# Kernel optimization log

Measured on AMD Instinct MI355X. Metric: run time of the kernel, lower is better.

## Reference

```python
import jax, jax.numpy as jnp
import numpy as np

E = 1024       # embed_dim
H = 16         # num_heads
HD = E // H    # head_dim = 64
ROPE = 32      # qk_rope_head_dim
NOPE = HD - ROPE  # 32
QR = 512       # q_lora_rank
KVR = 512      # kv_lora_rank
B, S = 1, 4096
EPS = 1e-5


def setup_inputs() -> dict:
    key = jax.random.key(0)
    ks = jax.random.split(key, 10)
    std = 0.02
    x = jax.random.normal(ks[0], (B, S, E), dtype=jnp.float32)
    mask = jnp.tril(jnp.ones((S, S), dtype=jnp.int32))  # causal decoder mask
    Wqa = jax.random.normal(ks[1], (QR, E), dtype=jnp.float32) * std
    qa_ln_w = jnp.ones((QR,), jnp.float32) + jax.random.normal(ks[2], (QR,), jnp.float32) * 0.01
    qa_ln_b = jax.random.normal(ks[3], (QR,), jnp.float32) * 0.01
    Wqb = jax.random.normal(ks[4], (H * HD, QR), dtype=jnp.float32) * std
    Wkva = jax.random.normal(ks[5], (KVR + ROPE, E), dtype=jnp.float32) * std
    kva_ln_w = jnp.ones((KVR,), jnp.float32) + jax.random.normal(ks[6], (KVR,), jnp.float32) * 0.01
    kva_ln_b = jax.random.normal(ks[7], (KVR,), jnp.float32) * 0.01
    Wkvb = jax.random.normal(ks[8], (H * (NOPE + HD), KVR), dtype=jnp.float32) * std
    Wo = jax.random.normal(ks[9], (E, H * HD), dtype=jnp.float32) * std
    return {"x": x, "mask": mask, "Wqa": Wqa, "qa_ln_w": qa_ln_w, "qa_ln_b": qa_ln_b,
            "Wqb": Wqb, "Wkva": Wkva, "kva_ln_w": kva_ln_w, "kva_ln_b": kva_ln_b,
            "Wkvb": Wkvb, "Wo": Wo}


def _layernorm(x, w, b):
    mu = jnp.mean(x, axis=-1, keepdims=True)
    var = jnp.var(x, axis=-1, keepdims=True)
    return (x - mu) * jax.lax.rsqrt(var + EPS) * w + b


def _rope_freqs(seq_len):
    inv_freq = 1.0 / (10000.0 ** (jnp.arange(0, ROPE, 2, dtype=jnp.float32) / ROPE))
    freqs = jnp.arange(seq_len, dtype=jnp.float32)[:, None] * inv_freq[None, :]  # [S, ROPE/2]
    return jnp.cos(freqs), jnp.sin(freqs)


def _apply_rope(x, cos, sin):
    # x: [B, S, h, ROPE] (interleaved-pair RoPE). cos/sin: [S, ROPE/2]
    x1 = x[..., ::2]
    x2 = x[..., 1::2]
    c = cos[None, :, None, :]
    s = sin[None, :, None, :]
    r1 = x1 * c - x2 * s
    r2 = x1 * s + x2 * c
    return jnp.stack([r1, r2], axis=-1).reshape(x.shape)


def reference(x, mask, Wqa, qa_ln_w, qa_ln_b, Wqb, Wkva, kva_ln_w, kva_ln_b, Wkvb, Wo):
    b, s, _ = x.shape
    # Q LoRA path
    q_c = _layernorm(x @ Wqa.T, qa_ln_w, qa_ln_b)          # [B,S,QR]
    q = (q_c @ Wqb.T).reshape(b, s, H, HD)                 # [B,S,H,HD]
    q_nope, q_pe = q[..., :NOPE], q[..., NOPE:]
    # KV LoRA path with decoupled rope channel
    kv = x @ Wkva.T                                        # [B,S,KVR+ROPE]
    ckv, k_pe = kv[..., :KVR], kv[..., KVR:]
    ckv = _layernorm(ckv, kva_ln_w, kva_ln_b)
    kv_dec = (ckv @ Wkvb.T).reshape(b, s, H, NOPE + HD)    # [B,S,H,NOPE+HD]
    k_nope, v = kv_dec[..., :NOPE], kv_dec[..., NOPE:]
    k_pe = k_pe.reshape(b, s, 1, ROPE)
    cos, sin = _rope_freqs(s)
    q_pe = _apply_rope(q_pe, cos, sin)
    k_pe = _apply_rope(k_pe, cos, sin)
    q_full = jnp.concatenate([q_nope, q_pe], axis=-1)      # [B,S,H,HD]
    k_full = jnp.concatenate([k_nope, jnp.broadcast_to(k_pe, (b, s, H, ROPE))], axis=-1)
    scale = 1.0 / np.sqrt(HD)
    scores = jnp.einsum('bqhd,bkhd->bhqk', q_full, k_full) * scale
    scores = jnp.where(mask[None, None, :, :] == 0, jnp.float32(-1e9), scores)
    p = jax.nn.softmax(scores, axis=-1)                    # dropout is identity (eval)
    out = jnp.einsum('bhqk,bkhd->bqhd', p, v).reshape(b, s, H * HD)
    return out @ Wo.T
```

## Files before the change

kernel.cpp:

```cpp
#include <hip/hip_runtime.h>
#include <hip/hip_bf16.h>
#include <stdint.h>


#define SLEN 4096
#define EDIM 1024
#define NH   16
#define NPAIR 160

typedef __attribute__((ext_vector_type(8))) short short8;
typedef __attribute__((ext_vector_type(4))) float f32x4;

__device__ __forceinline__ ushort f2bf(float f) {
  __hip_bfloat16 h = __float2bfloat16(f);
  ushort u; __builtin_memcpy(&u, &h, 2); return u;
}
__device__ __forceinline__ float bf2f(ushort u) {
  uint32_t x = (uint32_t)u << 16;
  float f; __builtin_memcpy(&f, &x, 4); return f;
}
__device__ __forceinline__ uint32_t cvt_pk_bf16(float lo, float hi) {
  uint32_t r;
  asm("v_cvt_pk_bf16_f32 %0, %1, %2" : "=v"(r) : "v"(lo), "v"(hi));
  return r;
}

#define GLD_LDS16(g, l) __builtin_amdgcn_global_load_lds(                      \
    (const __attribute__((address_space(1))) uint32_t*)(g),                    \
    (__attribute__((address_space(3))) uint32_t*)(l), 16, 0, 0)

struct CastSeg { const float4* src; ushort* dst; int n4; };
struct CastArgs { CastSeg seg[6]; int total4; };
__global__ void cast_all(CastArgs a) {
  int i = blockIdx.x * blockDim.x + threadIdx.x;
  int stride = gridDim.x * blockDim.x;
  for (; i < a.total4; i += stride) {
    int idx = i, s = 0;
    while (idx >= a.seg[s].n4) { idx -= a.seg[s].n4; ++s; }
    float4 v = a.seg[s].src[idx];
    ushort4 o;
    o.x = f2bf(v.x); o.y = f2bf(v.y); o.z = f2bf(v.z); o.w = f2bf(v.w);
    *(ushort4*)(a.seg[s].dst + (size_t)idx * 4) = o;
  }
}

__global__ void rope_table(float* __restrict__ cosT, float* __restrict__ sinT) {
  int idx = blockIdx.x * blockDim.x + threadIdx.x;
  if (idx >= SLEN * 16) return;
  int s = idx >> 4, i = idx & 15;
  float inv = expf(-((float)(2 * i) / 32.0f) * logf(10000.0f));
  float ang = (float)s * inv;
  cosT[idx] = cosf(ang);
  sinT[idx] = sinf(ang);
}

template <typename CT, bool ROPE, bool KVPACK>
__device__ __forceinline__ void gemm_body(
    ushort* As, ushort* Bs,
    const ushort* __restrict__ A, const ushort* __restrict__ B, CT* __restrict__ C,
    int M, int N, int K, int bx, int by,
    const float* __restrict__ cosT, const float* __restrict__ sinT,
    ushort* __restrict__ kf, ushort* __restrict__ vt) {
  const int tid = threadIdx.x;
  const int lane = tid & 63, wave = tid >> 6;
  const int bm = bx * 64, bn = by * 128;
  const int wm = (wave >> 1) * 32, wn = (wave & 1) * 64;

  f32x4 acc[2][4];
#pragma unroll
  for (int m = 0; m < 2; ++m)
#pragma unroll
    for (int n = 0; n < 4; ++n) acc[m][n] = (f32x4)0.0f;

  const int srow = lane >> 3;
  const int scb = (lane & 7) << 4;
  const int srcb = scb ^ ((srow & 7) << 4);

  auto stage = [&](int k0, int buf) {
#pragma unroll
    for (int c = 0; c < 2; ++c) {
      int r = wave * 16 + c * 8 + srow;
      const ushort* ga = A + (size_t)(bm + r) * K + k0 + (srcb >> 1);
      GLD_LDS16(ga, As + buf * 4096 + (wave * 16 + c * 8) * 64);
    }
#pragma unroll
    for (int c = 0; c < 4; ++c) {
      int r = wave * 32 + c * 8 + srow;
      int rb = bn + r; if (rb >= N) rb = N - 1;
      const ushort* gb = B + (size_t)rb * K + k0 + (srcb >> 1);
      GLD_LDS16(gb, Bs + buf * 8192 + (wave * 32 + c * 8) * 64);
    }
  };

  stage(0, 0);
  __syncthreads();
  int cur = 0;
  for (int k0 = 0; k0 < K; k0 += 64) {
    if (k0 + 64 < K) stage(k0 + 64, cur ^ 1);
    const char* Ab = (const char*)(As + cur * 4096);
    const char* Bb = (const char*)(Bs + cur * 8192);
#pragma unroll
    for (int kk = 0; kk < 2; ++kk) {
      short8 af[2], bf[4];
#pragma unroll
      for (int m = 0; m < 2; ++m) {
        int row = wm + m * 16 + (lane & 15);
        int cb = (kk * 64 + ((lane >> 4) << 4)) ^ ((row & 7) << 4);
        af[m] = *(const short8*)(Ab + row * 128 + cb);
      }
#pragma unroll
      for (int n = 0; n < 4; ++n) {
        int row = wn + n * 16 + (lane & 15);
        int cb = (kk * 64 + ((lane >> 4) << 4)) ^ ((row & 7) << 4);
        bf[n] = *(const short8*)(Bb + row * 128 + cb);
      }
#pragma unroll
      for (int m = 0; m < 2; ++m)
#pragma unroll
        for (int n = 0; n < 4; ++n)
          acc[m][n] = __builtin_amdgcn_mfma_f32_16x16x32_bf16(af[m], bf[n], acc[m][n], 0, 0, 0);
    }
    __syncthreads();
    cur ^= 1;
  }

  if constexpr (KVPACK) {
    ushort* T = Bs;
#pragma unroll
    for (int m = 0; m < 2; ++m) {
      int gm = bm + wm + m * 16 + ((lane >> 4) << 2);
#pragma unroll
      for (int n = 0; n < 4; ++n) {
        int gn = bn + wn + n * 16 + (lane & 15);
        int h = gn / 96, dd = gn - h * 96;
#pragma unroll
        for (int r = 0; r < 4; ++r) {
          float v = acc[m][n][r];
          int s = gm + r;
          if (dd < 32) {
            kf[(size_t)s * EDIM + h * 64 + dd] = f2bf(v);
          } else {
            int so = s & 63;
            int sp = ((so >> 4) & 1) * 32 + ((so >> 2) & 3) * 8 + ((so >> 5) & 1) * 4 + (so & 3);
            T[(gn - bn) * 68 + sp] = f2bf(v);
          }
        }
      }
    }
    __syncthreads();
    int c = tid >> 1, half = tid & 1;
    int gn2 = bn + c, h2 = gn2 / 96, dd2 = gn2 - h2 * 96;
    if (dd2 >= 32) {
      ushort* dst = vt + (size_t)(h2 * 64 + dd2 - 32) * SLEN + bm + half * 32;
      const ushort* src = T + c * 68 + half * 32;
#pragma unroll
      for (int j = 0; j < 32; j += 4)
        *(ushort4*)(dst + j) = *(const ushort4*)(src + j);
    }
  } else {
    const float SCQ = 0.125f * 1.44269504089f;
#pragma unroll
    for (int m = 0; m < 2; ++m) {
      int gm = bm + wm + m * 16 + ((lane >> 4) << 2);
#pragma unroll
      for (int n = 0; n < 4; ++n) {
        int gn = bn + wn + n * 16 + (lane & 15);
        if (gn < N) {
#pragma unroll
          for (int r = 0; r < 4; ++r) {
            float v = acc[m][n][r];
            if constexpr (ROPE) {
              float partner = __shfl_xor(v, 1);
              int d = gn & 63;
              if (d >= 32) {
                int s = gm + r, pidx = (d - 32) >> 1;
                float cc = cosT[(s << 4) + pidx], sn = sinT[(s << 4) + pidx];
                v = (gn & 1) ? (partner * sn + v * cc) : (v * cc - partner * sn);
              }
              v *= SCQ;
            }
            if constexpr (__is_same(CT, ushort))
              C[(size_t)(gm + r) * N + gn] = f2bf(v);
            else
              C[(size_t)(gm + r) * N + gn] = v;
          }
        }
      }
    }
  }
}

__global__ __launch_bounds__(256, 3) void gemm_f32k(
    const ushort* __restrict__ A, const ushort* __restrict__ B, float* __restrict__ C,
    int M, int N, int K) {
  __shared__ ushort As[2 * 64 * 64];
  __shared__ ushort Bs[2 * 128 * 64];
  gemm_body<float, false, false>(As, Bs, A, B, C, M, N, K, blockIdx.x, blockIdx.y,
                                 nullptr, nullptr, nullptr, nullptr);
}
__global__ __launch_bounds__(256, 3) void gemm_bf16k(
    const ushort* __restrict__ A, const ushort* __restrict__ B, ushort* __restrict__ C,
    int M, int N, int K) {
  __shared__ ushort As[2 * 64 * 64];
  __shared__ ushort Bs[2 * 128 * 64];
  gemm_body<ushort, false, false>(As, Bs, A, B, C, M, N, K, blockIdx.x, blockIdx.y,
                                  nullptr, nullptr, nullptr, nullptr);
}
__global__ __launch_bounds__(256, 3) void gemm_dual(
    const ushort* __restrict__ Aq, const ushort* __restrict__ Bq, ushort* __restrict__ Cq,
    const ushort* __restrict__ Ak, const ushort* __restrict__ Bk,
    ushort* __restrict__ kf, ushort* __restrict__ vt,
    const float* __restrict__ cosT, const float* __restrict__ sinT) {
  __shared__ ushort As[2 * 64 * 64];
  __shared__ ushort Bs[2 * 128 * 64];
  if (blockIdx.y < 8)
    gemm_body<ushort, true, false>(As, Bs, Aq, Bq, Cq, SLEN, 1024, 512,
                                   blockIdx.x, blockIdx.y, cosT, sinT, nullptr, nullptr);
  else
    gemm_body<ushort, false, true>(As, Bs, Ak, Bk, (ushort*)nullptr, SLEN, 1536, 512,
                                   blockIdx.x, blockIdx.y - 8, nullptr, nullptr, kf, vt);
}

__global__ __launch_bounds__(256) void ln_both(
    const ushort* __restrict__ qakv,
    const float* __restrict__ qa_w, const float* __restrict__ qa_b,
    const float* __restrict__ kva_w, const float* __restrict__ kva_b,
    ushort* __restrict__ qc, ushort* __restrict__ ckv,
    const float* __restrict__ cosT, const float* __restrict__ sinT,
    ushort* __restrict__ kf) {
  const int row = blockIdx.x & 4095;
  const bool iskv = blockIdx.x >= 4096;
  const int tid = threadIdx.x;
  const ushort* px = qakv + (size_t)row * 1056 + (iskv ? 512 : 0);
  const float* w = iskv ? kva_w : qa_w;
  const float* b = iskv ? kva_b : qa_b;
  ushort* out = (iskv ? ckv : qc) + (size_t)row * 512;
  float x0 = bf2f(px[tid]), x1 = bf2f(px[tid + 256]);
  float s = x0 + x1, sq = x0 * x0 + x1 * x1;
#pragma unroll
  for (int off = 32; off; off >>= 1) {
    s += __shfl_down(s, off);
    sq += __shfl_down(sq, off);
  }
  __shared__ float redS[4], redQ[4];
  __shared__ ushort kpeS[32];
  int wave = tid >> 6, lane = tid & 63;
  if (lane == 0) { redS[wave] = s; redQ[wave] = sq; }
  __syncthreads();
  float st = redS[0] + redS[1] + redS[2] + redS[3];
  float sqt = redQ[0] + redQ[1] + redQ[2] + redQ[3];
  float mean = st * (1.0f / 512.0f);
  float var = sqt * (1.0f / 512.0f) - mean * mean;
  float rstd = rsqrtf(var + 1e-5f);
  out[tid] = f2bf((x0 - mean) * rstd * w[tid] + b[tid]);
  out[tid + 256] = f2bf((x1 - mean) * rstd * w[tid + 256] + b[tid + 256]);
  if (iskv) {
    if (tid < 32) {
      int p = tid >> 1;
      float xa = bf2f(px[512 + 2 * p]), xb = bf2f(px[512 + 2 * p + 1]);
      float c = cosT[(row << 4) + p], sn = sinT[(row << 4) + p];
      float v = (tid & 1) ? (xa * sn + xb * c) : (xa * c - xb * sn);
      kpeS[tid] = f2bf(v);
    }
    __syncthreads();
    for (int t = tid; t < 512; t += 256) {
      int h = t >> 5, j = t & 31;
      kf[(size_t)row * EDIM + h * 64 + 32 + j] = kpeS[j];
    }
  }
}

__global__ __launch_bounds__(256, 5) void flash_part(
    const ushort* __restrict__ Qf, const ushort* __restrict__ Kf,
    const ushort* __restrict__ Vt, ushort* __restrict__ Opart, float* __restrict__ MLpart) {
  __shared__ ushort Klds[64 * 64];
  __shared__ ushort Vlds[64 * 64];
  const int tid = threadIdx.x, lane = tid & 63, wave = tid >> 6;
  const int h = blockIdx.x;
  const int p = NPAIR - 1 - blockIdx.y;
  int qb, ck;
  if (p < 16)      { qb = p;               ck = 0; }
  else if (p < 48) { int j = p - 16; qb = 16 + (j >> 1); ck = j & 1; }
  else if (p < 96) { int j = p - 48; qb = 32 + j / 3;    ck = j - 3 * (j / 3); }
  else             { int j = p - 96; qb = 48 + (j >> 2); ck = j & 3; }
  const int q0 = qb * 64;
  const int t0 = ck * 16;
  const int t1 = min(t0 + 16, qb + 1);

  short8 aq[2];
  {
    const ushort* qrow =
        Qf + (((size_t)(q0 + wave * 16 + (lane & 15)) * 16 + h) << 6) + ((lane >> 4) << 3);
    aq[0] = *(const short8*)qrow;
    aq[1] = *(const short8*)(qrow + 32);
  }
  f32x4 oacc[4];
#pragma unroll
  for (int nf = 0; nf < 4; ++nf) oacc[nf] = (f32x4)0.0f;
  float lacc = 0.0f, mrun = -1e30f;

  const int strow = wave * 16 + (lane >> 3);
  const int srcb = ((lane & 7) << 4) ^ (((lane >> 3) & 7) << 4);

  for (int kb = t0; kb < t1; ++kb) {
#pragma unroll
    for (int c = 0; c < 2; ++c) {
      int r = strow + c * 8;
      const ushort* gk = Kf + (((size_t)(kb * 64 + r) * 16 + h) << 6) + (srcb >> 1);
      GLD_LDS16(gk, &Klds[(wave * 16 + c * 8) * 64]);
      const ushort* gv = Vt + (size_t)(h * 64 + r) * SLEN + kb * 64 + (srcb >> 1);
      GLD_LDS16(gv, &Vlds[(wave * 16 + c * 8) * 64]);
    }
    __syncthreads();

    f32x4 sfr[4];
#pragma unroll
    for (int nf = 0; nf < 4; ++nf) sfr[nf] = (f32x4)0.0f;
#pragma unroll
    for (int kk = 0; kk < 2; ++kk) {
#pragma unroll
      for (int nf = 0; nf < 4; ++nf) {
        int row = nf * 16 + (lane & 15);
        int cb = (kk * 64 + ((lane >> 4) << 4)) ^ ((row & 7) << 4);
        short8 ak = *(const short8*)((const char*)Klds + row * 128 + cb);
        sfr[nf] = __builtin_amdgcn_mfma_f32_16x16x32_bf16(ak, aq[kk], sfr[nf], 0, 0, 0);
      }
    }
    if (kb == qb) {
      const int qloc = wave * 16 + (lane & 15);
      const int kg = (lane >> 4) << 2;
#pragma unroll
      for (int nf = 0; nf < 4; ++nf) {
#pragma unroll
        for (int r = 0; r < 4; ++r)
          if (nf * 16 + kg + r > qloc) sfr[nf][r] = -1e30f;
      }
    }
    float pm = -1e30f;
#pragma unroll
    for (int nf = 0; nf < 4; ++nf)
#pragma unroll
      for (int r = 0; r < 4; ++r) pm = fmaxf(pm, sfr[nf][r]);
    pm = fmaxf(pm, __shfl_xor(pm, 16));
    pm = fmaxf(pm, __shfl_xor(pm, 32));
    if (__any(pm > mrun + 8.0f)) {
      float mnew = fmaxf(mrun, pm);
      float corr = exp2f(mrun - mnew);
      mrun = mnew;
      lacc *= corr;
      const int gbase = lane & 48;
#pragma unroll
      for (int r = 0; r < 4; ++r) {
        float cB = __shfl(corr, gbase + ((lane >> 4) << 2) + r);
#pragma unroll
        for (int nf = 0; nf < 4; ++nf) oacc[nf][r] *= cB;
      }
    }
    float ps = 0.0f;
#pragma unroll
    for (int nf = 0; nf < 4; ++nf)
#pragma unroll
      for (int r = 0; r < 4; ++r) {
        float pv = exp2f(sfr[nf][r] - mrun);
        sfr[nf][r] = pv;
        ps += pv;
      }
    ps += __shfl_xor(ps, 16);
    ps += __shfl_xor(ps, 32);
    lacc += ps;
    short8 ap[2];
#pragma unroll
    for (int kk = 0; kk < 2; ++kk) {
      union { uint32_t u[4]; short8 s; } pk;
      pk.u[0] = cvt_pk_bf16(sfr[kk][0], sfr[kk][1]);
      pk.u[1] = cvt_pk_bf16(sfr[kk][2], sfr[kk][3]);
      pk.u[2] = cvt_pk_bf16(sfr[kk + 2][0], sfr[kk + 2][1]);
      pk.u[3] = cvt_pk_bf16(sfr[kk + 2][2], sfr[kk + 2][3]);
      ap[kk] = pk.s;
    }
#pragma unroll
    for (int nf = 0; nf < 4; ++nf) {
#pragma unroll
      for (int kk = 0; kk < 2; ++kk) {
        int row = nf * 16 + (lane & 15);
        int cb = (kk * 64 + ((lane >> 4) << 4)) ^ ((row & 7) << 4);
        short8 bv = *(const short8*)((const char*)Vlds + row * 128 + cb);
        oacc[nf] = __builtin_amdgcn_mfma_f32_16x16x32_bf16(ap[kk], bv, oacc[nf], 0, 0, 0);
      }
    }
    __syncthreads();
  }
  const size_t pb = (size_t)h * NPAIR + p;
#pragma unroll
  for (int nf = 0; nf < 4; ++nf) {
#pragma unroll
    for (int r = 0; r < 4; ++r) {
      int row = wave * 16 + ((lane >> 4) << 2) + r;
      int d = nf * 16 + (lane & 15);
      Opart[(pb * 64 + row) * 64 + d] = f2bf(oacc[nf][r]);
    }
  }
  if (lane < 16) {
    MLpart[pb * 128 + wave * 16 + lane] = mrun;
    MLpart[pb * 128 + 64 + wave * 16 + lane] = lacc;
  }
}

__global__ __launch_bounds__(256) void flash_combine(
    const ushort* __restrict__ Opart, const float* __restrict__ MLpart,
    ushort* __restrict__ attn) {
  const int qb = blockIdx.x, h = blockIdx.y;
  const int g = qb >> 4, n = g + 1;
  const int base = (g == 0 ? 0 : g == 1 ? 16 : g == 2 ? 48 : 96) + (qb - (g << 4)) * n;
  __shared__ float mS[4][64], lS[4][64];
  const int tid = threadIdx.x;
  for (int i = tid; i < n * 64; i += 256) {
    int part = i >> 6, row = i & 63;
    size_t pb = (size_t)h * NPAIR + base + part;
    mS[part][row] = MLpart[pb * 128 + row];
    lS[part][row] = MLpart[pb * 128 + 64 + row];
  }
  __syncthreads();
  const int d = tid & 63, rg = tid >> 6;
#pragma unroll 4
  for (int k = 0; k < 16; ++k) {
    int row = rg * 16 + k;
    float M = mS[0][row];
    for (int i = 1; i < n; ++i) M = fmaxf(M, mS[i][row]);
    float L = 0.0f, acc = 0.0f;
    for (int i = 0; i < n; ++i) {
      float w = exp2f(mS[i][row] - M);
      L += lS[i][row] * w;
      acc += bf2f(Opart[(((size_t)h * NPAIR + base + i) * 64 + row) * 64 + d]) * w;
    }
    attn[(size_t)(qb * 64 + row) * EDIM + h * 64 + d] = f2bf(acc / L);
  }
}

extern "C" void kernel_launch(void* const* d_in, const int* in_sizes, int n_in,
                              void* d_out, int out_size, void* d_ws, size_t ws_size,
                              hipStream_t stream) {
  const float* x     = (const float*)d_in[0];
  const float* Wqa   = (const float*)d_in[2];
  const float* qa_w  = (const float*)d_in[3];
  const float* qa_b  = (const float*)d_in[4];
  const float* Wqb   = (const float*)d_in[5];
  const float* Wkva  = (const float*)d_in[6];
  const float* kva_w = (const float*)d_in[7];
  const float* kva_b = (const float*)d_in[8];
  const float* Wkvb  = (const float*)d_in[9];
  const float* Wo    = (const float*)d_in[10];
  float* out = (float*)d_out;

  char* ws = (char*)d_ws;
  size_t off = 0;
  auto alloc = [&](size_t bytes) {
    char* p = ws + off;
    off += (bytes + 255) & ~(size_t)255;
    return p;
  };
  ushort* xb      = (ushort*)alloc((size_t)SLEN * EDIM * 2);
  ushort* wqkva_b = (ushort*)alloc((size_t)1056 * 1024 * 2);
  ushort* wqb_b   = (ushort*)alloc((size_t)1024 * 512 * 2);
  ushort* wkvb_b  = (ushort*)alloc((size_t)1536 * 512 * 2);
  ushort* wo_b    = (ushort*)alloc((size_t)1024 * 1024 * 2);
  float*  cosT    = (float*)alloc((size_t)SLEN * 16 * 4);
  float*  sinT    = (float*)alloc((size_t)SLEN * 16 * 4);
  ushort* qc_b    = (ushort*)alloc((size_t)SLEN * 512 * 2);
  ushort* qf_b    = (ushort*)alloc((size_t)SLEN * EDIM * 2);
  ushort* ckv_b   = (ushort*)alloc((size_t)SLEN * 512 * 2);
  ushort* kf_b    = (ushort*)alloc((size_t)SLEN * EDIM * 2);
  ushort* vt_b    = (ushort*)alloc((size_t)SLEN * EDIM * 2);
  ushort* attn_b  = (ushort*)alloc((size_t)SLEN * EDIM * 2);
  ushort* qakv_bf = (ushort*)alloc((size_t)SLEN * 1056 * 2);
  float*  MLpart  = (float*)alloc((size_t)NH * NPAIR * 128 * 4);
  ushort* Opart   = (ushort*)alloc((size_t)NH * NPAIR * 64 * 64 * 2);

  CastArgs ca;
  ca.seg[0] = { (const float4*)x,    xb,                               SLEN * EDIM / 4 };
  ca.seg[1] = { (const float4*)Wqa,  wqkva_b,                          512 * 1024 / 4 };
  ca.seg[2] = { (const float4*)Wkva, wqkva_b + (size_t)512 * 1024,     544 * 1024 / 4 };
  ca.seg[3] = { (const float4*)Wqb,  wqb_b,                            1024 * 512 / 4 };
  ca.seg[4] = { (const float4*)Wkvb, wkvb_b,                           1536 * 512 / 4 };
  ca.seg[5] = { (const float4*)Wo,   wo_b,                             1024 * 1024 / 4 };
  ca.total4 = ca.seg[0].n4 + ca.seg[1].n4 + ca.seg[2].n4 + ca.seg[3].n4 + ca.seg[4].n4 + ca.seg[5].n4;
  cast_all<<<dim3(2048), 256, 0, stream>>>(ca);
  rope_table<<<dim3((SLEN * 16 + 255) / 256), 256, 0, stream>>>(cosT, sinT);

  gemm_bf16k<<<dim3(64, 9), 256, 0, stream>>>(xb, wqkva_b, qakv_bf, SLEN, 1056, 1024);
  ln_both<<<dim3(8192), 256, 0, stream>>>(qakv_bf, qa_w, qa_b, kva_w, kva_b,
                                          qc_b, ckv_b, cosT, sinT, kf_b);
  gemm_dual<<<dim3(64, 20), 256, 0, stream>>>(qc_b, wqb_b, qf_b, ckv_b, wkvb_b,
                                              kf_b, vt_b, cosT, sinT);

  flash_part<<<dim3(NH, NPAIR), 256, 0, stream>>>(qf_b, kf_b, vt_b, Opart, MLpart);
  flash_combine<<<dim3(64, 16), 256, 0, stream>>>(Opart, MLpart, attn_b);
  gemm_f32k<<<dim3(64, 8), 256, 0, stream>>>(attn_b, wo_b, out, SLEN, 1024, 1024);

  (void)in_sizes; (void)n_in; (void)out_size; (void)ws_size;
}
```

Measured before the change: 177.0 us.

## Stage two KV tiles per barrier in flash_part and fold rope table into cast

The flash_part loop now loads two K/V tiles into doubled LDS buffers before each barrier and processes both, halving the number of barrier pairs per key block. Occupancy hint drops from 5 to 4 blocks per CU to fit the larger shared memory. Separately, the rope cos/sin table generation is merged into the cast kernel to remove one launch. The loads are still not overlapped with compute, so the gain relies on fewer syncs and more outstanding loads, at the cost of lower occupancy.

```diff
diff --git a/kernel.cpp b/kernel.cpp
--- a/kernel.cpp
+++ b/kernel.cpp
@@ -31,7 +31,15 @@
 
 struct CastSeg { const float4* src; ushort* dst; int n4; };
 struct CastArgs { CastSeg seg[6]; int total4; };
-__global__ void cast_all(CastArgs a) {
+__global__ void cast_all(CastArgs a, float* __restrict__ cosT, float* __restrict__ sinT) {
+  if (blockIdx.x < 256) {
+    int idx = blockIdx.x * 256 + threadIdx.x;
+    int s = idx >> 4, i = idx & 15;
+    float inv = expf(-((float)(2 * i) / 32.0f) * logf(10000.0f));
+    float ang = (float)s * inv;
+    cosT[idx] = cosf(ang);
+    sinT[idx] = sinf(ang);
+  }
   int i = blockIdx.x * blockDim.x + threadIdx.x;
   int stride = gridDim.x * blockDim.x;
   for (; i < a.total4; i += stride) {
@@ -42,16 +50,6 @@
     o.x = f2bf(v.x); o.y = f2bf(v.y); o.z = f2bf(v.z); o.w = f2bf(v.w);
     *(ushort4*)(a.seg[s].dst + (size_t)idx * 4) = o;
   }
-}
-
-__global__ void rope_table(float* __restrict__ cosT, float* __restrict__ sinT) {
-  int idx = blockIdx.x * blockDim.x + threadIdx.x;
-  if (idx >= SLEN * 16) return;
-  int s = idx >> 4, i = idx & 15;
-  float inv = expf(-((float)(2 * i) / 32.0f) * logf(10000.0f));
-  float ang = (float)s * inv;
-  cosT[idx] = cosf(ang);
-  sinT[idx] = sinf(ang);
 }
 
 template <typename CT, bool ROPE, bool KVPACK>
@@ -270,11 +268,11 @@
   }
 }
 
-__global__ __launch_bounds__(256, 5) void flash_part(
+__global__ __launch_bounds__(256, 4) void flash_part(
     const ushort* __restrict__ Qf, const ushort* __restrict__ Kf,
     const ushort* __restrict__ Vt, ushort* __restrict__ Opart, float* __restrict__ MLpart) {
-  __shared__ ushort Klds[64 * 64];
-  __shared__ ushort Vlds[64 * 64];
+  __shared__ ushort Klds[2][64 * 64];
+  __shared__ ushort Vlds[2][64 * 64];
   const int tid = threadIdx.x, lane = tid & 63, wave = tid >> 6;
   const int h = blockIdx.x;
   const int p = NPAIR - 1 - blockIdx.y;
@@ -302,17 +300,18 @@
   const int strow = wave * 16 + (lane >> 3);
   const int srcb = ((lane & 7) << 4) ^ (((lane >> 3) & 7) << 4);
 
-  for (int kb = t0; kb < t1; ++kb) {
+  auto stage = [&](int kb, int buf) {
 #pragma unroll
     for (int c = 0; c < 2; ++c) {
       int r = strow + c * 8;
       const ushort* gk = Kf + (((size_t)(kb * 64 + r) * 16 + h) << 6) + (srcb >> 1);
-      GLD_LDS16(gk, &Klds[(wave * 16 + c * 8) * 64]);
+      GLD_LDS16(gk, &Klds[buf][(wave * 16 + c * 8) * 64]);
       const ushort* gv = Vt + (size_t)(h * 64 + r) * SLEN + kb * 64 + (srcb >> 1);
-      GLD_LDS16(gv, &Vlds[(wave * 16 + c * 8) * 64]);
-    }
-    __syncthreads();
-
+      GLD_LDS16(gv, &Vlds[buf][(wave * 16 + c * 8) * 64]);
+    }
+  };
+
+  auto process = [&](int buf, int kb) {
     f32x4 sfr[4];
 #pragma unroll
     for (int nf = 0; nf < 4; ++nf) sfr[nf] = (f32x4)0.0f;
@@ -322,7 +321,7 @@
       for (int nf = 0; nf < 4; ++nf) {
         int row = nf * 16 + (lane & 15);
         int cb = (kk * 64 + ((lane >> 4) << 4)) ^ ((row & 7) << 4);
-        short8 ak = *(const short8*)((const char*)Klds + row * 128 + cb);
+        short8 ak = *(const short8*)((const char*)&Klds[buf][0] + row * 128 + cb);
         sfr[nf] = __builtin_amdgcn_mfma_f32_16x16x32_bf16(ak, aq[kk], sfr[nf], 0, 0, 0);
       }
     }
@@ -384,11 +383,22 @@
       for (int kk = 0; kk < 2; ++kk) {
         int row = nf * 16 + (lane & 15);
         int cb = (kk * 64 + ((lane >> 4) << 4)) ^ ((row & 7) << 4);
-        short8 bv = *(const short8*)((const char*)Vlds + row * 128 + cb);
+        short8 bv = *(const short8*)((const char*)&Vlds[buf][0] + row * 128 + cb);
         oacc[nf] = __builtin_amdgcn_mfma_f32_16x16x32_bf16(ap[kk], bv, oacc[nf], 0, 0, 0);
       }
     }
+  };
+
+  int kb = t0;
+  while (kb < t1) {
+    const int nt = min(2, t1 - kb);
+    stage(kb, 0);
+    if (nt == 2) stage(kb + 1, 1);
     __syncthreads();
+    process(0, kb);
+    if (nt == 2) process(1, kb + 1);
+    __syncthreads();
+    kb += nt;
   }
   const size_t pb = (size_t)h * NPAIR + p;
 #pragma unroll
@@ -484,8 +494,7 @@
   ca.seg[4] = { (const float4*)Wkvb, wkvb_b,                           1536 * 512 / 4 };
   ca.seg[5] = { (const float4*)Wo,   wo_b,                             1024 * 1024 / 4 };
   ca.total4 = ca.seg[0].n4 + ca.seg[1].n4 + ca.seg[2].n4 + ca.seg[3].n4 + ca.seg[4].n4 + ca.seg[5].n4;
-  cast_all<<<dim3(2048), 256, 0, stream>>>(ca);
-  rope_table<<<dim3((SLEN * 16 + 255) / 256), 256, 0, stream>>>(cosT, sinT);
+  cast_all<<<dim3(2048), 256, 0, stream>>>(ca, cosT, sinT);
 
   gemm_bf16k<<<dim3(64, 9), 256, 0, stream>>>(xb, wqkva_b, qakv_bf, SLEN, 1056, 1024);
   ln_both<<<dim3(8192), 256, 0, stream>>>(qakv_bf, qa_w, qa_b, kva_w, kva_b,
```

New measurement: 176.5 us. About the same (-0.3%).
